# Optimization experiments

Measured on AMD Instinct MI355X. Metric: run time of the kernel, lower is better.

The kernel has to match this reference:

```python
import jax, jax.numpy as jnp
import numpy as np

N_LOC = 20000
N_EXP = 200000
H = 64
E = 1500000
L = 400000


def setup_inputs() -> dict:
    key = jax.random.key(0)
    ks = jax.random.split(key, 24)
    f = jnp.float32
    w = lambda k, shp: jax.random.normal(k, shp, dtype=f) * 0.1
    # edges: ('location','of','experts'): src in [0,N_LOC), dst in [0,N_EXP)
    src = jax.random.randint(ks[0], (E,), 0, N_LOC)
    dst = jax.random.randint(ks[1], (E,), 0, N_EXP)
    edge_of = jnp.stack([src, dst])          # location -> experts
    edge_rev = jnp.stack([dst, src])         # experts -> location (ToUndirected)
    row = jax.random.randint(ks[2], (L,), 0, N_LOC)
    col = jax.random.randint(ks[3], (L,), 0, N_EXP)
    edge_label_index = jnp.stack([row, col])
    return dict(
        emb_loc=w(ks[4], (N_LOC, H)), emb_exp=w(ks[5], (N_EXP, H)),
        W1l_of=w(ks[6], (H, H)), b1_of=jnp.zeros((H,), f), W1r_of=w(ks[7], (H, H)),
        W1l_rev=w(ks[8], (H, H)), b1_rev=jnp.zeros((H,), f), W1r_rev=w(ks[9], (H, H)),
        W2l_of=w(ks[10], (H, H)), b2_of=jnp.zeros((H,), f), W2r_of=w(ks[11], (H, H)),
        W2l_rev=w(ks[12], (H, H)), b2_rev=jnp.zeros((H,), f), W2r_rev=w(ks[13], (H, H)),
        dW1=w(ks[14], (2 * H, H)), db1=jnp.zeros((H,), f),
        dW2=w(ks[15], (H, 1)), db2=jnp.zeros((1,), f),
        edge_of=edge_of, edge_rev=edge_rev, edge_label_index=edge_label_index,
    )


def _sage(x_src, x_dst, edge, Wl, b, Wr, n_dst):
    # PyG SAGEConv: lin_l(mean of neighbor msgs) + lin_r(x_dst); bias only in lin_l
    s, d = edge[0], edge[1]
    msg = x_src[s]                                   # [E, H] gather
    summed = jax.ops.segment_sum(msg, d, num_segments=n_dst)
    cnt = jax.ops.segment_sum(jnp.ones((edge.shape[1],), x_src.dtype), d, num_segments=n_dst)
    agg = summed / jnp.maximum(cnt, 1.0)[:, None]
    return agg @ Wl + b + x_dst @ Wr


def reference(emb_loc, emb_exp,
              W1l_of, b1_of, W1r_of, W1l_rev, b1_rev, W1r_rev,
              W2l_of, b2_of, W2r_of, W2l_rev, b2_rev, W2r_rev,
              dW1, db1, dW2, db2,
              edge_of, edge_rev, edge_label_index):
    # layer 1 (to_hetero: one conv per edge type; each dst type has one incoming type)
    z_exp = jax.nn.relu(_sage(emb_loc, emb_exp, edge_of, W1l_of, b1_of, W1r_of, N_EXP))
    z_loc = jax.nn.relu(_sage(emb_exp, emb_loc, edge_rev, W1l_rev, b1_rev, W1r_rev, N_LOC))
    # layer 2 (no relu)
    z_exp2 = _sage(z_loc, z_exp, edge_of, W2l_of, b2_of, W2r_of, N_EXP)
    z_loc2 = _sage(z_exp, z_loc, edge_rev, W2l_rev, b2_rev, W2r_rev, N_LOC)
    # EdgeDecoder: gather-concat-MLP
    row, col = edge_label_index[0], edge_label_index[1]
    z = jnp.concatenate([z_loc2[row], z_exp2[col]], axis=-1)  # [L, 2H]
    h = jax.nn.relu(z @ dW1 + db1)
    out = (h @ dW2 + db2).reshape(-1)
    return out
```

## Files before the change

kernel.cpp:

```cpp
#include <hip/hip_runtime.h>

#define H 64
#define NE 1500000
#define NLOC 20000
#define NEXP 200000
#define NL 400000
#define PAD_E 32
#define PAD_L 128

#define EB 896
#define NBE 224
#define LB 112
#define NBL 179
#define BIN_CHUNK 2048
#define NBIN ((NE + BIN_CHUNK - 1) / BIN_CHUNK)
#define EBSLOT 28
#define LBSLOT 32
#define ECAP 8192
#define LCAP 10240
#define FCAP 4096

#define WS_NEED 90546112ULL

typedef int vint4 __attribute__((ext_vector_type(4)));
typedef _Float16 f16x8 __attribute__((ext_vector_type(8)));
typedef float f32x4 __attribute__((ext_vector_type(4)));
typedef unsigned int u32;
typedef unsigned short u16;
typedef unsigned long long u64;

__device__ __forceinline__ float bcastf(float v, int k) {
  return __int_as_float(__builtin_amdgcn_readlane(__float_as_int(v), k));
}
__device__ __forceinline__ int bcasti(int v, int k) {
  return __builtin_amdgcn_readlane(v, k);
}

__global__ __launch_bounds__(256) void bin_kernel(
    const int* __restrict__ src, const int* __restrict__ dst,
    u32* __restrict__ expQ, u32* __restrict__ locQ,
    int* __restrict__ qcnt, int* __restrict__ flbk_cnt,
    u64* __restrict__ flbkQ)
{
  __shared__ u32 eb[NBE * EBSLOT];
  __shared__ u32 lb[NBL * LBSLOT];
  __shared__ int ec[NBE], lc[NBL], ebase[NBE], lbase[NBL];

  const int tid = threadIdx.x;
  for (int i = tid; i < NBE; i += 256) ec[i] = 0;
  for (int i = tid; i < NBL; i += 256) lc[i] = 0;
  __syncthreads();

  const long base = (long)blockIdx.x * BIN_CHUNK + tid * 8;
  if (base < NE) {
    vint4 s0 = __builtin_nontemporal_load((const vint4*)(src + base));
    vint4 s1 = __builtin_nontemporal_load((const vint4*)(src + base + 4));
    vint4 d0 = __builtin_nontemporal_load((const vint4*)(dst + base));
    vint4 d1 = __builtin_nontemporal_load((const vint4*)(dst + base + 4));
    int ss[8] = {s0.x, s0.y, s0.z, s0.w, s1.x, s1.y, s1.z, s1.w};
    int dd[8] = {d0.x, d0.y, d0.z, d0.w, d1.x, d1.y, d1.z, d1.w};
#pragma unroll
    for (int k = 0; k < 8; k++) {
      const u32 d = (u32)dd[k], s = (u32)ss[k];
      {
        const u32 b = d / (u32)EB;
        const int pos = atomicAdd(&ec[b], 1);
        if (pos < EBSLOT) {
          eb[b * EBSLOT + pos] = ((d - b * EB) << 16) | s;
        } else {
          int fi = atomicAdd(flbk_cnt, 1);
          if (fi < FCAP) flbkQ[fi] = ((u64)d << 32) | (u64)s;
        }
      }
      {
        const u32 b = s / (u32)LB;
        const int pos = atomicAdd(&lc[b], 1);
        if (pos < LBSLOT) {
          lb[b * LBSLOT + pos] = ((s - b * LB) << 18) | d;
        } else {
          int fi = atomicAdd(flbk_cnt, 1);
          if (fi < FCAP) flbkQ[fi] = (1ULL << 63) | ((u64)s << 32) | (u64)d;
        }
      }
    }
  }
  __syncthreads();

  for (int i = tid; i < NBE; i += 256) {
    const int c = min(ec[i], EBSLOT);
    ebase[i] = c ? atomicAdd(&qcnt[i], c) : 0;
  }
  for (int i = tid; i < NBL; i += 256) {
    const int c = min(lc[i], LBSLOT);
    lbase[i] = c ? atomicAdd(&qcnt[NBE + i], c) : 0;
  }
  __syncthreads();

  const int wid = tid >> 6, ln = tid & 63;
  for (int b = wid; b < NBE; b += 4) {
    const int c = min(ec[b], EBSLOT);
    if (ln < c) {
      const int idx = ebase[b] + ln;
      const u32 r = eb[b * EBSLOT + ln];
      if (idx < ECAP) {
        expQ[(long)b * ECAP + idx] = r;
      } else {
        int fi = atomicAdd(flbk_cnt, 1);
        if (fi < FCAP)
          flbkQ[fi] = ((u64)(b * EB + (r >> 16)) << 32) | (u64)(r & 0xFFFF);
      }
    }
  }
  for (int b = wid; b < NBL; b += 4) {
    const int c = min(lc[b], LBSLOT);
    if (ln < c) {
      const int idx = lbase[b] + ln;
      const u32 r = lb[b * LBSLOT + ln];
      if (idx < LCAP) {
        locQ[(long)b * LCAP + idx] = r;
      } else {
        int fi = atomicAdd(flbk_cnt, 1);
        if (fi < FCAP)
          flbkQ[fi] = (1ULL << 63) | ((u64)(b * LB + (r >> 18)) << 32) |
                      (u64)(r & 0x3FFFF);
      }
    }
  }
}

__global__ __launch_bounds__(256) void build_kernel(
    const u32* __restrict__ expQ, const u32* __restrict__ locQ,
    const int* __restrict__ qcnt,
    u16* __restrict__ nbr_exp, int* __restrict__ nbr_loc,
    int* __restrict__ cnt_exp, int* __restrict__ cnt_loc)
{
  __shared__ char ldsraw[60928];
  const int tid = threadIdx.x;
  if (blockIdx.x < NBE) {
    const int b = blockIdx.x;
    u16* rows = (u16*)ldsraw;
    int* cnts = (int*)(ldsraw + 57344);
    for (int i = tid; i < EB; i += 256) cnts[i] = 0;
    __syncthreads();
    const int n = min(qcnt[b], ECAP);
    for (int i = tid; i < n; i += 256) {
      const u32 r = expQ[(long)b * ECAP + i];
      const int nl = (int)(r >> 16);
      const int pos = atomicAdd(&cnts[nl], 1);
      if (pos < PAD_E) rows[nl * PAD_E + pos] = (u16)(r & 0xFFFF);
    }
    __syncthreads();
    const int node0 = b * EB;
    const int nn = min(EB, NEXP - node0);
    u32* grows = (u32*)(nbr_exp + (long)node0 * PAD_E);
    const u32* lrows = (const u32*)rows;
    for (int j = tid; j < nn * (PAD_E / 2); j += 256) grows[j] = lrows[j];
    for (int i = tid; i < nn; i += 256) cnt_exp[node0 + i] = cnts[i];
  } else {
    const int b = blockIdx.x - NBE;
    int* rows = (int*)ldsraw;
    int* cnts = (int*)(ldsraw + 57344);
    for (int i = tid; i < LB; i += 256) cnts[i] = 0;
    __syncthreads();
    const int n = min(qcnt[NBE + b], LCAP);
    for (int i = tid; i < n; i += 256) {
      const u32 r = locQ[(long)b * LCAP + i];
      const int sl = (int)(r >> 18);
      const int pos = atomicAdd(&cnts[sl], 1);
      if (pos < PAD_L) rows[sl * PAD_L + pos] = (int)(r & 0x3FFFF);
    }
    __syncthreads();
    const int node0 = b * LB;
    const int nn = min(LB, NLOC - node0);
    int* grows = nbr_loc + (long)node0 * PAD_L;
    for (int j = tid; j < nn * PAD_L; j += 256) grows[j] = rows[j];
    for (int i = tid; i < nn; i += 256) cnt_loc[node0 + i] = cnts[i];
  }
}

__global__ __launch_bounds__(256) void fold_kernel(
    const float* __restrict__ W2r_of, const float* __restrict__ W2l_of,
    const float* __restrict__ W2l_rev, const float* __restrict__ W2r_rev,
    const float* __restrict__ dW1, const float* __restrict__ b2_of,
    const float* __restrict__ b2_rev,
    float* __restrict__ Wf_q, float* __restrict__ Wf_y2,
    float* __restrict__ Wf_t2, float* __restrict__ Wf_p,
    float* __restrict__ bf_q, float* __restrict__ bf_p,
    const int* __restrict__ flbk_cnt, const u64* __restrict__ flbkQ,
    u16* __restrict__ nbr_exp, int* __restrict__ nbr_loc,
    int* __restrict__ cnt_exp, int* __restrict__ cnt_loc)
{
  const int lane = threadIdx.x & 63;
  const int w = threadIdx.x >> 6;
  const float* dW1a = dW1;
  const float* dW1b = dW1 + H * H;
  if (blockIdx.x < 4) {
    const float* A; const float* B; float* C;
    switch (blockIdx.x) {
      case 0:  A = W2r_of;  B = dW1b; C = Wf_q;  break;
      case 1:  A = W2l_of;  B = dW1b; C = Wf_y2; break;
      case 2:  A = W2l_rev; B = dW1a; C = Wf_t2; break;
      default: A = W2r_rev; B = dW1a; C = Wf_p;  break;
    }
    float b[H];
#pragma unroll
    for (int k = 0; k < H; k++) b[k] = B[k * H + lane];
    for (int r = w * 16; r < w * 16 + 16; r++) {
      const float xv = A[r * H + lane];
      float a0 = 0.f, a1 = 0.f;
#pragma unroll
      for (int k = 0; k < H; k += 2) {
        a0 += bcastf(xv, k)     * b[k];
        a1 += bcastf(xv, k + 1) * b[k + 1];
      }
      C[r * H + lane] = a0 + a1;
    }
  } else if (blockIdx.x == 4) {
    if (w < 2) {
      const float* bv_src = (w == 0) ? b2_of : b2_rev;
      const float* B      = (w == 0) ? dW1b  : dW1a;
      float* o            = (w == 0) ? bf_q  : bf_p;
      float wk[H];
#pragma unroll
      for (int k = 0; k < H; k++) wk[k] = B[k * H + lane];
      const float bv = bv_src[lane];
      float a = 0.f;
#pragma unroll
      for (int k = 0; k < H; k++) a += bcastf(bv, k) * wk[k];
      o[lane] = a;
    }
  } else {
    const int n = min(*flbk_cnt, FCAP);
    for (int i = threadIdx.x; i < n; i += 256) {
      const u64 rec = flbkQ[i];
      const int node = (int)((rec >> 32) & 0x3FFFF);
      const int val  = (int)(rec & 0x3FFFF);
      if ((rec >> 63) == 0) {
        int pos = atomicAdd(&cnt_exp[node], 1);
        if (pos < PAD_E) nbr_exp[(long)node * PAD_E + pos] = (u16)val;
      } else {
        int pos = atomicAdd(&cnt_loc[node], 1);
        if (pos < PAD_L) nbr_loc[(long)node * PAD_L + pos] = val;
      }
    }
  }
}

__global__ __launch_bounds__(256, 4) void dense_linear_kernel(
    const float* __restrict__ x, _Float16* __restrict__ out16,
    const float* __restrict__ W, int n)
{
  const int lane = threadIdx.x & 63;
  const int gw = (blockIdx.x * 256 + threadIdx.x) >> 6;
  const int nw = (gridDim.x * 256) >> 6;
  float w[H];
#pragma unroll
  for (int k = 0; k < H; k++) w[k] = W[k * H + lane];
  for (int i = gw; i < n; i += nw) {
    const float xv = x[i * H + lane];
    float a0 = 0.f, a1 = 0.f;
#pragma unroll
    for (int k = 0; k < H; k += 2) {
      a0 += bcastf(xv, k)     * w[k];
      a1 += bcastf(xv, k + 1) * w[k + 1];
    }
    out16[i * H + lane] = (_Float16)(a0 + a1);
  }
}

__global__ __launch_bounds__(256, 4) void mfma_pass_kernel(
    const unsigned short* __restrict__ nbr, const int* __restrict__ cnt,
    const _Float16* __restrict__ y,
    const float* a32, const _Float16* a16,
    _Float16* out1, const float* __restrict__ W1,
    const float* __restrict__ bias, int relu,
    _Float16* out2, const float* __restrict__ W2)
{
  const int w = threadIdx.x >> 6;
  const int lane = threadIdx.x & 63;
  const int q = lane >> 4;
  const int cidx = lane & 15;
  const int rb = blockIdx.x * 16;

  __shared__ float Gs[16 * H];

  f16x8 b1lo, b1hi, b2lo, b2hi;
#pragma unroll
  for (int j = 0; j < 8; j++) {
    b1lo[j] = (_Float16)W1[(q * 8 + j) * H + w * 16 + cidx];
    b1hi[j] = (_Float16)W1[(32 + q * 8 + j) * H + w * 16 + cidx];
  }
  if (out2) {
#pragma unroll
    for (int j = 0; j < 8; j++) {
      b2lo[j] = (_Float16)W2[(q * 8 + j) * H + w * 16 + cidx];
      b2hi[j] = (_Float16)W2[(32 + q * 8 + j) * H + w * 16 + cidx];
    }
  }

  if (y) {
    for (int rr = 0; rr < 4; rr++) {
      const int i = rb + w * 4 + rr;
      const int c = cnt[i];
      const int cc = min(c, PAD_E);
      const unsigned short* nb = nbr + (long)i * PAD_E;
      float s0 = 0.f, s1 = 0.f, s2 = 0.f, s3 = 0.f;
      const int id = (lane < cc) ? (int)nb[lane] : 0;
      int k = 0;
      const int m4 = cc & ~3;
      for (; k < m4; k += 4) {
        const int i0 = bcasti(id, k), i1 = bcasti(id, k + 1),
                  i2 = bcasti(id, k + 2), i3 = bcasti(id, k + 3);
        s0 += (float)y[(long)i0 * H + lane];
        s1 += (float)y[(long)i1 * H + lane];
        s2 += (float)y[(long)i2 * H + lane];
        s3 += (float)y[(long)i3 * H + lane];
      }
      for (; k < cc; k++) s0 += (float)y[(long)bcasti(id, k) * H + lane];
      Gs[(w * 4 + rr) * H + lane] =
          ((s0 + s1) + (s2 + s3)) / fmaxf((float)c, 1.0f);
    }
  }

  f16x8 a0, a1;
  if (a16) {
    const _Float16* ar = a16 + (long)(rb + cidx) * H;
    a0 = *(const f16x8*)(ar + q * 8);
    a1 = *(const f16x8*)(ar + 32 + q * 8);
  } else {
    const float* ar = a32 + (long)(rb + cidx) * H;
#pragma unroll
    for (int j = 0; j < 8; j++) {
      a0[j] = (_Float16)ar[q * 8 + j];
      a1[j] = (_Float16)ar[32 + q * 8 + j];
    }
  }
  f32x4 acc1 = {0.f, 0.f, 0.f, 0.f};
  acc1 = __builtin_amdgcn_mfma_f32_16x16x32_f16(a0, b1lo, acc1, 0, 0, 0);
  acc1 = __builtin_amdgcn_mfma_f32_16x16x32_f16(a1, b1hi, acc1, 0, 0, 0);
  f32x4 acc2 = {0.f, 0.f, 0.f, 0.f};
  if (out2) {
    acc2 = __builtin_amdgcn_mfma_f32_16x16x32_f16(a0, b2lo, acc2, 0, 0, 0);
    acc2 = __builtin_amdgcn_mfma_f32_16x16x32_f16(a1, b2hi, acc2, 0, 0, 0);
  }

  const float bj = bias ? bias[w * 16 + cidx] : 0.f;
  __syncthreads();
#pragma unroll
  for (int reg = 0; reg < 4; reg++) {
    const int r = q * 4 + reg;
    float v = acc1[reg] + bj;
    if (y) v += Gs[r * H + w * 16 + cidx];
    if (relu) v = fmaxf(v, 0.f);
    out1[(long)(rb + r) * H + w * 16 + cidx] = (_Float16)v;
    if (out2)
      out2[(long)(rb + r) * H + w * 16 + cidx] = (_Float16)acc2[reg];
  }
}

__global__ __launch_bounds__(256, 4) void loc_gather_kernel(
    const int* __restrict__ nbr, const int* __restrict__ cnt,
    const _Float16* __restrict__ T, const float* __restrict__ x,
    float* __restrict__ out32, _Float16* __restrict__ out16,
    const float* __restrict__ Wr, const float* __restrict__ bias,
    int n, int relu)
{
  const int lane = threadIdx.x & 63;
  const int gw = (blockIdx.x * 256 + threadIdx.x) >> 6;
  const int nw = (gridDim.x * 256) >> 6;
  float wr[H];
#pragma unroll
  for (int k = 0; k < H; k++) wr[k] = Wr[k * H + lane];
  const float bj = bias[lane];
  for (int i = gw; i < n; i += nw) {
    const int c = cnt[i];
    const int cc = min(c, PAD_L);
    const int* nb = nbr + (long)i * PAD_L;
    float s0 = 0.f, s1 = 0.f, s2 = 0.f, s3 = 0.f;
    int e = 0;
    while (e < cc) {
      const int m = min(cc - e, 64);
      const int id = (lane < m) ? nb[e + lane] : 0;
      int k = 0;
      const int m4 = m & ~3;
      for (; k < m4; k += 4) {
        const int i0 = bcasti(id, k), i1 = bcasti(id, k + 1),
                  i2 = bcasti(id, k + 2), i3 = bcasti(id, k + 3);
        s0 += (float)T[(long)i0 * H + lane];
        s1 += (float)T[(long)i1 * H + lane];
        s2 += (float)T[(long)i2 * H + lane];
        s3 += (float)T[(long)i3 * H + lane];
      }
      for (; k < m; k++) s0 += (float)T[(long)bcasti(id, k) * H + lane];
      e += m;
    }
    const float agg = ((s0 + s1) + (s2 + s3)) / fmaxf((float)c, 1.0f);
    const float xv = x[i * H + lane];
    float a0 = 0.f, a1 = 0.f;
#pragma unroll
    for (int k = 0; k < H; k += 2) {
      a0 += bcastf(xv, k)     * wr[k];
      a1 += bcastf(xv, k + 1) * wr[k + 1];
    }
    float acc = agg + bj + a0 + a1;
    if (relu) acc = fmaxf(acc, 0.0f);
    if (out32) out32[i * H + lane] = acc;
    else       out16[i * H + lane] = (_Float16)acc;
  }
}

__global__ __launch_bounds__(256, 4) void edge_kernel(
    const int* __restrict__ row, const int* __restrict__ col,
    const _Float16* __restrict__ P, const _Float16* __restrict__ Q,
    const float* __restrict__ db1, const float* __restrict__ dW2,
    const float* __restrict__ db2, float* __restrict__ out)
{
  const int lane = threadIdx.x & 63;
  const int gw = (blockIdx.x * 256 + threadIdx.x) >> 6;
  const int nw = (gridDim.x * 256) >> 6;
  const float bj = db1[lane];
  const float w2 = dW2[lane];
  const float b2 = db2[0];
  for (int e = gw * 4; e < NL; e += nw * 4) {
    const int n4 = min(NL - e, 4);
    float h[4];
#pragma unroll
    for (int k = 0; k < 4; k++) {
      if (k < n4) {
        const int r = row[e + k], c = col[e + k];
        const float p = (float)P[(long)r * H + lane];
        const float q = (float)Q[(long)c * H + lane];
        h[k] = fmaxf(p + q + bj, 0.0f) * w2;
      } else h[k] = 0.f;
    }
#pragma unroll
    for (int off = 1; off < 64; off <<= 1) {
#pragma unroll
      for (int k = 0; k < 4; k++) h[k] += __shfl_xor(h[k], off);
    }
    if (lane == 0) {
#pragma unroll
      for (int k = 0; k < 4; k++)
        if (k < n4) out[e + k] = h[k] + b2;
    }
  }
}

extern "C" void kernel_launch(void* const* d_in, const int* in_sizes, int n_in,
                              void* d_out, int out_size, void* d_ws, size_t ws_size,
                              hipStream_t stream) {
  const float* emb_loc = (const float*)d_in[0];
  const float* emb_exp = (const float*)d_in[1];
  const float* W1l_of  = (const float*)d_in[2];
  const float* b1_of   = (const float*)d_in[3];
  const float* W1r_of  = (const float*)d_in[4];
  const float* W1l_rev = (const float*)d_in[5];
  const float* b1_rev  = (const float*)d_in[6];
  const float* W1r_rev = (const float*)d_in[7];
  const float* W2l_of  = (const float*)d_in[8];
  const float* b2_of   = (const float*)d_in[9];
  const float* W2r_of  = (const float*)d_in[10];
  const float* W2l_rev = (const float*)d_in[11];
  const float* b2_rev  = (const float*)d_in[12];
  const float* W2r_rev = (const float*)d_in[13];
  const float* dW1     = (const float*)d_in[14];
  const float* db1     = (const float*)d_in[15];
  const float* dW2     = (const float*)d_in[16];
  const float* db2     = (const float*)d_in[17];
  const int*   edge_of = (const int*)d_in[18];
  const int*   eli     = (const int*)d_in[20];

  const int* src = edge_of;
  const int* dst = edge_of + NE;
  const int* row = eli;
  const int* col = eli + NL;

  if (ws_size < WS_NEED) return;

  char* ws = (char*)d_ws;
  int*            cnt_loc = (int*)(ws);
  int*            cnt_exp = (int*)(ws + 80000);
  int*            nbr_loc = (int*)(ws + 880064);
  unsigned short* nbr_exp = (unsigned short*)(ws + 11120064);
  _Float16*       Ylh     = (_Float16*)(ws + 23920064);
  _Float16*       Y2fh    = (_Float16*)(ws + 26480064);
  float*          z_loc   = (float*)(ws + 29040064);
  _Float16*       PH      = (_Float16*)(ws + 34160064);
  _Float16*       ZE      = (_Float16*)(ws + 39280064);
  _Float16*       TH      = (_Float16*)(ws + 64880064);
  u32*            expQ    = (u32*)(ws + 64880064);
  u32*            locQ    = (u32*)(ws + 72220096);
  int*            qcnt    = (int*)(ws + 79551936);
  int*            flbk    = (int*)(ws + 79553552);
  u64*            flbkQ   = (u64*)(ws + 79554048);
  float*          Wf_q    = (float*)(ws + 90480064);
  float*          Wf_y2   = (float*)(ws + 90496448);
  float*          Wf_t2   = (float*)(ws + 90512832);
  float*          Wf_p    = (float*)(ws + 90529216);
  float*          bf_q    = (float*)(ws + 90545600);
  float*          bf_p    = (float*)(ws + 90545856);
  float*          out     = (float*)d_out;

  (void)hipMemsetAsync(ws + 79551936, 0, 2048, stream);

  bin_kernel<<<NBIN, 256, 0, stream>>>(src, dst, expQ, locQ, qcnt, flbk, flbkQ);
  build_kernel<<<NBE + NBL, 256, 0, stream>>>(expQ, locQ, qcnt,
      nbr_exp, nbr_loc, cnt_exp, cnt_loc);
  fold_kernel<<<6, 256, 0, stream>>>(W2r_of, W2l_of, W2l_rev, W2r_rev,
                                     dW1, b2_of, b2_rev,
                                     Wf_q, Wf_y2, Wf_t2, Wf_p, bf_q, bf_p,
                                     flbk, flbkQ, nbr_exp, nbr_loc,
                                     cnt_exp, cnt_loc);

  dense_linear_kernel<<<1280, 256, 0, stream>>>(emb_loc, Ylh, W1l_of, NLOC);
  mfma_pass_kernel<<<NEXP / 16, 256, 0, stream>>>(nbr_exp, cnt_exp, Ylh,
      emb_exp, (const _Float16*)nullptr, ZE, W1r_of, b1_of, 1, TH, W1l_rev);
  loc_gather_kernel<<<1250, 256, 0, stream>>>(nbr_loc, cnt_loc, TH,
      emb_loc, z_loc, (_Float16*)nullptr, W1r_rev, b1_rev, NLOC, 1);

  dense_linear_kernel<<<1280, 256, 0, stream>>>(z_loc, Y2fh, Wf_y2, NLOC);
  mfma_pass_kernel<<<NEXP / 16, 256, 0, stream>>>(nbr_exp, cnt_exp, Y2fh,
      (const float*)nullptr, ZE, ZE, Wf_q, bf_q, 0, TH, Wf_t2);
  loc_gather_kernel<<<1250, 256, 0, stream>>>(nbr_loc, cnt_loc, TH,
      z_loc, (float*)nullptr, PH, Wf_p, bf_p, NLOC, 0);

  edge_kernel<<<2048, 256, 0, stream>>>(row, col, PH, ZE,
                                        db1, dW2, db2, out);
}
```

Measured before the change: 527.1 us.

## Fuse first dense linear into prep kernel and tune gather kernels

Merges the first emb_loc @ W1l_of dense linear into the weight-folding/fallback prep kernel, removing one launch. In the MFMA pass it loads the A operand before the gather, using vectorized float4 loads, batches the count and neighbor-index loads across the four rows, and pads the shared staging buffer to 68 floats per row to avoid bank conflicts. The loc gather loop is unrolled by eight with more accumulators, and its grid grows from 1250 to 2048 blocks. The added register pressure and the extra blocks in the prep launch may offset some of the benefit.

```diff
diff --git a/kernel.cpp b/kernel.cpp
--- a/kernel.cpp
+++ b/kernel.cpp
@@ -178,7 +178,7 @@
   }
 }
 
-__global__ __launch_bounds__(256) void fold_kernel(
+__global__ __launch_bounds__(256) void prep_kernel(
     const float* __restrict__ W2r_of, const float* __restrict__ W2l_of,
     const float* __restrict__ W2l_rev, const float* __restrict__ W2r_rev,
     const float* __restrict__ dW1, const float* __restrict__ b2_of,
@@ -188,7 +188,9 @@
     float* __restrict__ bf_q, float* __restrict__ bf_p,
     const int* __restrict__ flbk_cnt, const u64* __restrict__ flbkQ,
     u16* __restrict__ nbr_exp, int* __restrict__ nbr_loc,
-    int* __restrict__ cnt_exp, int* __restrict__ cnt_loc)
+    int* __restrict__ cnt_exp, int* __restrict__ cnt_loc,
+    const float* __restrict__ emb_loc, _Float16* __restrict__ Ylh,
+    const float* __restrict__ W1l_of)
 {
   const int lane = threadIdx.x & 63;
   const int w = threadIdx.x >> 6;
@@ -229,7 +231,7 @@
       for (int k = 0; k < H; k++) a += bcastf(bv, k) * wk[k];
       o[lane] = a;
     }
-  } else {
+  } else if (blockIdx.x == 5) {
     const int n = min(*flbk_cnt, FCAP);
     for (int i = threadIdx.x; i < n; i += 256) {
       const u64 rec = flbkQ[i];
@@ -243,6 +245,21 @@
         if (pos < PAD_L) nbr_loc[(long)node * PAD_L + pos] = val;
       }
     }
+  } else {
+    float wreg[H];
+#pragma unroll
+    for (int k = 0; k < H; k++) wreg[k] = W1l_of[k * H + lane];
+    const int gw2 = (blockIdx.x - 6) * 4 + w;
+    for (int r = gw2; r < NLOC; r += 5000) {
+      const float xv = emb_loc[(long)r * H + lane];
+      float a0 = 0.f, a1 = 0.f;
+#pragma unroll
+      for (int k = 0; k < H; k += 2) {
+        a0 += bcastf(xv, k)     * wreg[k];
+        a1 += bcastf(xv, k + 1) * wreg[k + 1];
+      }
+      Ylh[(long)r * H + lane] = (_Float16)(a0 + a1);
+    }
   }
 }
 
@@ -269,7 +286,7 @@
 }
 
 __global__ __launch_bounds__(256, 4) void mfma_pass_kernel(
-    const unsigned short* __restrict__ nbr, const int* __restrict__ cnt,
+    const u16* __restrict__ nbr, const int* __restrict__ cnt,
     const _Float16* __restrict__ y,
     const float* a32, const _Float16* a16,
     _Float16* out1, const float* __restrict__ W1,
@@ -282,7 +299,7 @@
   const int cidx = lane & 15;
   const int rb = blockIdx.x * 16;
 
-  __shared__ float Gs[16 * H];
+  __shared__ float Gs[16 * 68];
 
   f16x8 b1lo, b1hi, b2lo, b2hi;
 #pragma unroll
@@ -298,14 +315,42 @@
     }
   }
 
+  f16x8 a0, a1;
+  if (a16) {
+    const _Float16* ar = a16 + (long)(rb + cidx) * H;
+    a0 = *(const f16x8*)(ar + q * 8);
+    a1 = *(const f16x8*)(ar + 32 + q * 8);
+  } else {
+    const float* ar = a32 + (long)(rb + cidx) * H;
+    f32x4 v0 = *(const f32x4*)(ar + q * 8);
+    f32x4 v1 = *(const f32x4*)(ar + q * 8 + 4);
+    f32x4 v2 = *(const f32x4*)(ar + 32 + q * 8);
+    f32x4 v3 = *(const f32x4*)(ar + 32 + q * 8 + 4);
+#pragma unroll
+    for (int j = 0; j < 4; j++) {
+      a0[j] = (_Float16)v0[j];
+      a0[j + 4] = (_Float16)v1[j];
+      a1[j] = (_Float16)v2[j];
+      a1[j + 4] = (_Float16)v3[j];
+    }
+  }
+
   if (y) {
+    const int i0r = rb + w * 4;
+    int c4[4];
+#pragma unroll
+    for (int rr = 0; rr < 4; rr++) c4[rr] = cnt[i0r + rr];
+    int id4[4];
+#pragma unroll
     for (int rr = 0; rr < 4; rr++) {
-      const int i = rb + w * 4 + rr;
-      const int c = cnt[i];
-      const int cc = min(c, PAD_E);
-      const unsigned short* nb = nbr + (long)i * PAD_E;
+      const int c = min(c4[rr], PAD_E);
+      id4[rr] = (lane < c) ? (int)nbr[(long)(i0r + rr) * PAD_E + lane] : 0;
+    }
+#pragma unroll
+    for (int rr = 0; rr < 4; rr++) {
+      const int cc = min(c4[rr], PAD_E);
+      const int id = id4[rr];
       float s0 = 0.f, s1 = 0.f, s2 = 0.f, s3 = 0.f;
-      const int id = (lane < cc) ? (int)nb[lane] : 0;
       int k = 0;
       const int m4 = cc & ~3;
       for (; k < m4; k += 4) {
@@ -317,24 +362,11 @@
         s3 += (float)y[(long)i3 * H + lane];
       }
       for (; k < cc; k++) s0 += (float)y[(long)bcasti(id, k) * H + lane];
-      Gs[(w * 4 + rr) * H + lane] =
-          ((s0 + s1) + (s2 + s3)) / fmaxf((float)c, 1.0f);
-    }
-  }
-
-  f16x8 a0, a1;
-  if (a16) {
-    const _Float16* ar = a16 + (long)(rb + cidx) * H;
-    a0 = *(const f16x8*)(ar + q * 8);
-    a1 = *(const f16x8*)(ar + 32 + q * 8);
-  } else {
-    const float* ar = a32 + (long)(rb + cidx) * H;
-#pragma unroll
-    for (int j = 0; j < 8; j++) {
-      a0[j] = (_Float16)ar[q * 8 + j];
-      a1[j] = (_Float16)ar[32 + q * 8 + j];
-    }
-  }
+      Gs[(w * 4 + rr) * 68 + lane] =
+          ((s0 + s1) + (s2 + s3)) / fmaxf((float)c4[rr], 1.0f);
+    }
+  }
+
   f32x4 acc1 = {0.f, 0.f, 0.f, 0.f};
   acc1 = __builtin_amdgcn_mfma_f32_16x16x32_f16(a0, b1lo, acc1, 0, 0, 0);
   acc1 = __builtin_amdgcn_mfma_f32_16x16x32_f16(a1, b1hi, acc1, 0, 0, 0);
@@ -350,7 +382,7 @@
   for (int reg = 0; reg < 4; reg++) {
     const int r = q * 4 + reg;
     float v = acc1[reg] + bj;
-    if (y) v += Gs[r * H + w * 16 + cidx];
+    if (y) v += Gs[r * 68 + w * 16 + cidx];
     if (relu) v = fmaxf(v, 0.f);
     out1[(long)(rb + r) * H + w * 16 + cidx] = (_Float16)v;
     if (out2)
@@ -377,11 +409,27 @@
     const int cc = min(c, PAD_L);
     const int* nb = nbr + (long)i * PAD_L;
     float s0 = 0.f, s1 = 0.f, s2 = 0.f, s3 = 0.f;
+    float s4 = 0.f, s5 = 0.f, s6 = 0.f, s7 = 0.f;
     int e = 0;
     while (e < cc) {
       const int m = min(cc - e, 64);
       const int id = (lane < m) ? nb[e + lane] : 0;
       int k = 0;
+      const int m8 = m & ~7;
+      for (; k < m8; k += 8) {
+        const int i0 = bcasti(id, k),     i1 = bcasti(id, k + 1),
+                  i2 = bcasti(id, k + 2), i3 = bcasti(id, k + 3),
+                  i4 = bcasti(id, k + 4), i5 = bcasti(id, k + 5),
+                  i6 = bcasti(id, k + 6), i7 = bcasti(id, k + 7);
+        s0 += (float)T[(long)i0 * H + lane];
+        s1 += (float)T[(long)i1 * H + lane];
+        s2 += (float)T[(long)i2 * H + lane];
+        s3 += (float)T[(long)i3 * H + lane];
+        s4 += (float)T[(long)i4 * H + lane];
+        s5 += (float)T[(long)i5 * H + lane];
+        s6 += (float)T[(long)i6 * H + lane];
+        s7 += (float)T[(long)i7 * H + lane];
+      }
       const int m4 = m & ~3;
       for (; k < m4; k += 4) {
         const int i0 = bcasti(id, k), i1 = bcasti(id, k + 1),
@@ -394,8 +442,9 @@
       for (; k < m; k++) s0 += (float)T[(long)bcasti(id, k) * H + lane];
       e += m;
     }
-    const float agg = ((s0 + s1) + (s2 + s3)) / fmaxf((float)c, 1.0f);
-    const float xv = x[i * H + lane];
+    const float agg = (((s0 + s1) + (s2 + s3)) + ((s4 + s5) + (s6 + s7))) /
+                      fmaxf((float)c, 1.0f);
+    const float xv = x[(long)i * H + lane];
     float a0 = 0.f, a1 = 0.f;
 #pragma unroll
     for (int k = 0; k < H; k += 2) {
@@ -404,8 +453,8 @@
     }
     float acc = agg + bj + a0 + a1;
     if (relu) acc = fmaxf(acc, 0.0f);
-    if (out32) out32[i * H + lane] = acc;
-    else       out16[i * H + lane] = (_Float16)acc;
+    if (out32) out32[(long)i * H + lane] = acc;
+    else       out16[(long)i * H + lane] = (_Float16)acc;
   }
 }
 
@@ -506,22 +555,22 @@
   bin_kernel<<<NBIN, 256, 0, stream>>>(src, dst, expQ, locQ, qcnt, flbk, flbkQ);
   build_kernel<<<NBE + NBL, 256, 0, stream>>>(expQ, locQ, qcnt,
       nbr_exp, nbr_loc, cnt_exp, cnt_loc);
-  fold_kernel<<<6, 256, 0, stream>>>(W2r_of, W2l_of, W2l_rev, W2r_rev,
-                                     dW1, b2_of, b2_rev,
-                                     Wf_q, Wf_y2, Wf_t2, Wf_p, bf_q, bf_p,
-                                     flbk, flbkQ, nbr_exp, nbr_loc,
-                                     cnt_exp, cnt_loc);
-
-  dense_linear_kernel<<<1280, 256, 0, stream>>>(emb_loc, Ylh, W1l_of, NLOC);
+  prep_kernel<<<1256, 256, 0, stream>>>(W2r_of, W2l_of, W2l_rev, W2r_rev,
+                                        dW1, b2_of, b2_rev,
+                                        Wf_q, Wf_y2, Wf_t2, Wf_p, bf_q, bf_p,
+                                        flbk, flbkQ, nbr_exp, nbr_loc,
+                                        cnt_exp, cnt_loc,
+                                        emb_loc, Ylh, W1l_of);
+
   mfma_pass_kernel<<<NEXP / 16, 256, 0, stream>>>(nbr_exp, cnt_exp, Ylh,
       emb_exp, (const _Float16*)nullptr, ZE, W1r_of, b1_of, 1, TH, W1l_rev);
-  loc_gather_kernel<<<1250, 256, 0, stream>>>(nbr_loc, cnt_loc, TH,
+  loc_gather_kernel<<<2048, 256, 0, stream>>>(nbr_loc, cnt_loc, TH,
       emb_loc, z_loc, (_Float16*)nullptr, W1r_rev, b1_rev, NLOC, 1);
 
   dense_linear_kernel<<<1280, 256, 0, stream>>>(z_loc, Y2fh, Wf_y2, NLOC);
   mfma_pass_kernel<<<NEXP / 16, 256, 0, stream>>>(nbr_exp, cnt_exp, Y2fh,
       (const float*)nullptr, ZE, ZE, Wf_q, bf_q, 0, TH, Wf_t2);
-  loc_gather_kernel<<<1250, 256, 0, stream>>>(nbr_loc, cnt_loc, TH,
+  loc_gather_kernel<<<2048, 256, 0, stream>>>(nbr_loc, cnt_loc, TH,
       z_loc, (float*)nullptr, PH, Wf_p, bf_p, NLOC, 0);
 
   edge_kernel<<<2048, 256, 0, stream>>>(row, col, PH, ZE,
```

Result: faster. 513.1 us (-2.7%).
